# Kernel optimization log

Measured on AMD Instinct MI355X. Metric: run time of the kernel, lower is better.

The kernel has to match this reference:

```python
import jax, jax.numpy as jnp
import numpy as np

N_NODES = 500_000
N_EDGES = 1_000_000
N_GRAPHS = 5_000
NUM_SHAPES = 16
NUM_COLORS = 16
NUM_REL = 3
NUM_CLASS = 10


def setup_inputs() -> dict:
    key = jax.random.key(0)
    ks = jax.random.split(key, 16)
    s = 0.1
    inp = {
        "x": jax.random.randint(ks[0], (N_NODES, 2), 0, NUM_SHAPES, dtype=jnp.int32),
        "edge_index": jax.random.randint(ks[1], (2, N_EDGES), 0, N_NODES, dtype=jnp.int32),
        "edge_type": jax.random.randint(ks[2], (N_EDGES,), 0, NUM_REL, dtype=jnp.int32),
        "ptr": jnp.arange(0, N_NODES + 1, N_NODES // N_GRAPHS, dtype=jnp.int32),  # [G+1]
        "shape_emb": jax.random.normal(ks[3], (NUM_SHAPES, 8), jnp.float32) * s,
        "color_emb": jax.random.normal(ks[4], (NUM_COLORS, 8), jnp.float32) * s,
        "pre_w": jax.random.normal(ks[5], (16, 32), jnp.float32) * s,
        "pre_b": jnp.zeros((32,), jnp.float32),
        "w1_rel": jax.random.normal(ks[6], (NUM_REL, 32, 64), jnp.float32) * s,
        "w1_root": jax.random.normal(ks[7], (32, 64), jnp.float32) * s,
        "b1": jnp.zeros((64,), jnp.float32),
        "w2_rel": jax.random.normal(ks[8], (NUM_REL, 64, 64), jnp.float32) * s,
        "w2_root": jax.random.normal(ks[9], (64, 64), jnp.float32) * s,
        "b2": jnp.zeros((64,), jnp.float32),
        "cls_w": jax.random.normal(ks[10], (64, NUM_CLASS), jnp.float32) * s,
        "cls_b": jnp.zeros((NUM_CLASS,), jnp.float32),
    }
    return inp


def rgcn_layer(h, w_rel, w_root, b, src, dst, etype):
    # PyG RGCNConv: out_i = bias + x_i @ root + sum_r mean_{j in N_r(i)} x_j @ W_r
    n = h.shape[0]
    hr = jnp.einsum('ni,rio->rno', h, w_rel)          # [R, N, F_out]: per-relation transform
    msg = hr[etype, src]                              # [E, F_out]: gather per-edge message
    seg = etype * n + dst                             # relation-separated segment ids
    agg = jax.ops.segment_sum(msg, seg, num_segments=NUM_REL * n)
    cnt = jax.ops.segment_sum(jnp.ones((msg.shape[0],), h.dtype), seg, num_segments=NUM_REL * n)
    agg = (agg / jnp.maximum(cnt, 1.0)[:, None]).reshape(NUM_REL, n, -1).sum(0)
    return agg + h @ w_root + b


def reference(x, edge_index, edge_type, ptr, shape_emb, color_emb, pre_w, pre_b,
              w1_rel, w1_root, b1, w2_rel, w2_root, b2, cls_w, cls_b):
    src, dst = edge_index[0], edge_index[1]
    h = jnp.concatenate([shape_emb[x[:, 0]], color_emb[x[:, 1]]], axis=1)  # [N,16]
    h = jax.nn.relu(h @ pre_w + pre_b)                                     # [N,32]
    h = jax.nn.relu(rgcn_layer(h, w1_rel, w1_root, b1, src, dst, edge_type))
    h = jax.nn.relu(rgcn_layer(h, w2_rel, w2_root, b2, src, dst, edge_type))
    last_idx = ptr[1:] - 1                                                 # [G]
    return h[last_idx] @ cls_w + cls_b                                     # [G, num_class]
```

## Files before the change

### kernel.cpp

```cpp
#include <hip/hip_runtime.h>

#define NB     64
#define CS     16
#define CAP1   32768
#define BC1    (CAP1 / NB)
#define ROWCAP 20
#define PMASK  0xFFFFF
#define CTRB(b) ((b) * CS)

__device__ __forceinline__ int bittest(const unsigned* bm, int n) {
    return (bm[n >> 5] >> (n & 31)) & 1u;
}

__device__ __forceinline__ void claim1(int n, int* __restrict__ slot1,
                                       int* __restrict__ ctr, int bucket,
                                       const int* __restrict__ x,
                                       int* __restrict__ snode) {
    if (atomicCAS(&slot1[n], -1, -2) == -1) {
        int p = atomicAdd(&ctr[CTRB(bucket)], 1);
        if (p < BC1) {
            int sl = bucket * BC1 + p;
            snode[sl] = x[2 * n] | (x[2 * n + 1] << 4);
            atomicExch(&slot1[n], sl);
        }
    }
}

__global__ void scan1_k(const int* __restrict__ src, const int* __restrict__ dst,
                        const int* __restrict__ et, const int* __restrict__ x,
                        int* __restrict__ slot1, int* __restrict__ snode,
                        int* __restrict__ pgE, int* __restrict__ ecnt2,
                        unsigned* __restrict__ bitN1, int* __restrict__ ctr,
                        int nE, int G, unsigned long long M, int stride) {
    int tid = blockIdx.x * blockDim.x + threadIdx.x;
    int nT  = gridDim.x * blockDim.x;
    for (int g = tid; g < G; g += nT) {
        int last = (g + 1) * stride - 1;
        atomicOr(&bitN1[last >> 5], 1u << (last & 31));
        claim1(last, slot1, ctr, g & (NB - 1), x, snode);
    }
    int bucket = (tid >> 6) & (NB - 1);
    int nC = (nE + 3) >> 2;
    for (int c = tid; c < nC; c += nT) {
        int e0 = c * 4;
        int d[4];
        int cnt = min(4, nE - e0);
        if (cnt == 4) { int4 v = *(const int4*)(dst + e0); d[0]=v.x; d[1]=v.y; d[2]=v.z; d[3]=v.w; }
        else for (int k = 0; k < cnt; k++) d[k] = dst[e0 + k];
#pragma unroll
        for (int k = 0; k < 4; k++) {
            if (k >= cnt) break;
            unsigned dk = (unsigned)d[k];
            unsigned q = (unsigned)(((unsigned long long)dk * M) >> 42);
            if ((int)(dk - q * (unsigned)stride) == stride - 1) {
                int e = e0 + k;
                int s = src[e], r = et[e];
                int idx = atomicAdd(&ecnt2[q], 1);
                if (idx < ROWCAP) pgE[q * ROWCAP + idx] = s | (r << 20);
                atomicOr(&bitN1[s >> 5], 1u << (s & 31));
                claim1(s, slot1, ctr, bucket, x, snode);
            }
        }
    }
}

__global__ void scan2_k(const int* __restrict__ src, const int* __restrict__ dst,
                        const int* __restrict__ et, const int* __restrict__ x,
                        const unsigned* __restrict__ bitN1,
                        const int* __restrict__ slot1, int* __restrict__ psE,
                        int* __restrict__ ecnt1, int nE) {
    int tid = blockIdx.x * blockDim.x + threadIdx.x;
    int nT  = gridDim.x * blockDim.x;
    int nC = (nE + 3) >> 2;
    for (int c = tid; c < nC; c += nT) {
        int e0 = c * 4;
        int d[4];
        int cnt = min(4, nE - e0);
        if (cnt == 4) { int4 v = *(const int4*)(dst + e0); d[0]=v.x; d[1]=v.y; d[2]=v.z; d[3]=v.w; }
        else for (int k = 0; k < cnt; k++) d[k] = dst[e0 + k];
#pragma unroll
        for (int k = 0; k < 4; k++) {
            if (k >= cnt) break;
            if (bittest(bitN1, d[k])) {
                int e = e0 + k;
                int s1 = slot1[d[k]];
                if (s1 >= 0) {
                    int s = src[e];
                    int pk = et[e] | (x[2 * s] << 4) | (x[2 * s + 1] << 8);
                    int idx = atomicAdd(&ecnt1[s1], 1);
                    if (idx < ROWCAP) psE[s1 * ROWCAP + idx] = pk;
                }
            }
        }
    }
}

__device__ __forceinline__ float h0_of(int x0, int x1, int fh,
        const float* __restrict__ s_se, const float* __restrict__ s_ce,
        const float* __restrict__ s_pw, const float* __restrict__ s_pb) {
    float h0 = s_pb[fh];
#pragma unroll
    for (int k = 0; k < 8; k++)
        h0 += s_se[x0 * 8 + k] * s_pw[k * 32 + fh] +
              s_ce[x1 * 8 + k] * s_pw[(k + 8) * 32 + fh];
    return fmaxf(h0, 0.f);
}

__device__ __forceinline__ void edge_acc(int pk, int fh,
        const float* __restrict__ s_se, const float* __restrict__ s_ce,
        const float* __restrict__ s_pw, const float* __restrict__ s_pb,
        float& a0, float& a1, float& a2, int& c0, int& c1, int& c2) {
    int r = pk & 15, x0 = (pk >> 4) & 15, x1 = (pk >> 8) & 15;
    float h0 = h0_of(x0, x1, fh, s_se, s_ce, s_pw, s_pb);
    if (r == 0)      { a0 += h0; c0++; }
    else if (r == 1) { a1 += h0; c1++; }
    else             { a2 += h0; c2++; }
}

__global__ __launch_bounds__(256, 2) void h1_k(
        const int* __restrict__ snode, const int* __restrict__ psE,
        const int* __restrict__ ecnt1, const int* __restrict__ ctr,
        const float* __restrict__ se, const float* __restrict__ ce,
        const float* __restrict__ pw, const float* __restrict__ pb,
        const float* __restrict__ w1r, const float* __restrict__ wroot1,
        const float* __restrict__ b1, float* __restrict__ h1buf) {
    __shared__ float smem[9056];
    int t = threadIdx.x;
    for (int i = t; i < 6144; i += 256) smem[i] = w1r[i];
    for (int i = t; i < 2048; i += 256) smem[6144 + i] = wroot1[i];
    if (t < 128) { smem[8192 + t] = se[t]; smem[8320 + t] = ce[t]; }
    for (int i = t; i < 512; i += 256) smem[8448 + i] = pw[i];
    if (t < 32) smem[8960 + t] = pb[t];
    if (t < 64) smem[8992 + t] = b1[t];
    __syncthreads();
    const float* s_w1  = smem;
    const float* s_wr1 = smem + 6144;
    const float* s_se  = smem + 8192;
    const float* s_ce  = smem + 8320;
    const float* s_pw  = smem + 8448;
    const float* s_pb  = smem + 8960;
    const float* s_b1  = smem + 8992;
    int f = t & 63, fh = f & 31;
    int wv  = (blockIdx.x * blockDim.x + t) >> 6;
    int nwv = (gridDim.x * blockDim.x) >> 6;
    int b   = wv & (NB - 1);
    int nj  = nwv >> 6;
    int cnt = min(ctr[CTRB(b)], BC1);
    for (int p = wv >> 6; p < cnt; p += nj) {
        int sl = b * BC1 + p;
        int sx = snode[sl];
        int m  = min(ecnt1[sl], ROWCAP);
        int base = sl * ROWCAP;
        float a0 = 0.f, a1 = 0.f, a2 = 0.f;
        int c0 = 0, c1 = 0, c2 = 0;
        if (m > 0) {
            int4 v = *(const int4*)(psE + base);
            edge_acc(v.x, fh, s_se, s_ce, s_pw, s_pb, a0, a1, a2, c0, c1, c2);
            if (m > 1) edge_acc(v.y, fh, s_se, s_ce, s_pw, s_pb, a0, a1, a2, c0, c1, c2);
            if (m > 2) edge_acc(v.z, fh, s_se, s_ce, s_pw, s_pb, a0, a1, a2, c0, c1, c2);
            if (m > 3) edge_acc(v.w, fh, s_se, s_ce, s_pw, s_pb, a0, a1, a2, c0, c1, c2);
            for (int e = 4; e < m; e++)
                edge_acc(psE[base + e], fh, s_se, s_ce, s_pw, s_pb, a0, a1, a2, c0, c1, c2);
        }
        float h0n = h0_of(sx & 15, (sx >> 4) & 15, fh, s_se, s_ce, s_pw, s_pb);
        float acc = s_b1[f];
        for (int k = 0; k < 32; k++)
            acc += __shfl(h0n, k, 64) * s_wr1[k * 64 + f];
        if (c0) {
            a0 *= 1.0f / (float)c0;
            for (int k = 0; k < 32; k++) acc += __shfl(a0, k, 64) * s_w1[k * 64 + f];
        }
        if (c1) {
            a1 *= 1.0f / (float)c1;
            for (int k = 0; k < 32; k++) acc += __shfl(a1, k, 64) * s_w1[2048 + k * 64 + f];
        }
        if (c2) {
            a2 *= 1.0f / (float)c2;
            for (int k = 0; k < 32; k++) acc += __shfl(a2, k, 64) * s_w1[4096 + k * 64 + f];
        }
        h1buf[sl * 64 + f] = fmaxf(acc, 0.f);
    }
}

__global__ __launch_bounds__(256, 2) void final_k(
        const int* __restrict__ slot1, const float* __restrict__ h1buf,
        const float* __restrict__ w2r, const float* __restrict__ wroot2,
        const float* __restrict__ b2, const float* __restrict__ cw,
        const float* __restrict__ cb, const int* __restrict__ pgE,
        const int* __restrict__ ecnt2, float* __restrict__ out,
        int G, int stride) {
    __shared__ float smem[12944];
    int t = threadIdx.x;
    for (int i = t; i < 12288; i += 256) smem[i] = w2r[i];
    for (int i = t; i < 640; i += 256) smem[12288 + i] = cw[i];
    if (t < 16) smem[12928 + t] = (t < 10) ? cb[t] : 0.f;
    __syncthreads();
    const float* s_w2 = smem;
    const float* s_cw = smem + 12288;
    const float* s_cb = smem + 12928;
    int f = t & 63;
    int g = (blockIdx.x * blockDim.x + t) >> 6;
    if (g >= G) return;
    int last = (g + 1) * stride - 1;
    int sll = slot1[last];
    float hlast = (sll >= 0) ? h1buf[sll * 64 + f] : 0.f;
    int m2 = min(ecnt2[g], ROWCAP);
    float a0 = 0.f, a1 = 0.f, a2 = 0.f;
    int c0 = 0, c1 = 0, c2 = 0;
    if (m2 > 0) {
        int4 v = *(const int4*)(pgE + g * ROWCAP);
        int q0 = slot1[v.x & PMASK];
        int q1 = (m2 > 1) ? slot1[v.y & PMASK] : -1;
        int q2 = (m2 > 2) ? slot1[v.z & PMASK] : -1;
        int q3 = (m2 > 3) ? slot1[v.w & PMASK] : -1;
        float h0v = (q0 >= 0) ? h1buf[q0 * 64 + f] : 0.f;
        float h1v = (q1 >= 0) ? h1buf[q1 * 64 + f] : 0.f;
        float h2v = (q2 >= 0) ? h1buf[q2 * 64 + f] : 0.f;
        float h3v = (q3 >= 0) ? h1buf[q3 * 64 + f] : 0.f;
        { int r = v.x >> 20;
          if (r == 0) { a0 += h0v; c0++; } else if (r == 1) { a1 += h0v; c1++; } else { a2 += h0v; c2++; } }
        if (m2 > 1) { int r = v.y >> 20;
          if (r == 0) { a0 += h1v; c0++; } else if (r == 1) { a1 += h1v; c1++; } else { a2 += h1v; c2++; } }
        if (m2 > 2) { int r = v.z >> 20;
          if (r == 0) { a0 += h2v; c0++; } else if (r == 1) { a1 += h2v; c1++; } else { a2 += h2v; c2++; } }
        if (m2 > 3) { int r = v.w >> 20;
          if (r == 0) { a0 += h3v; c0++; } else if (r == 1) { a1 += h3v; c1++; } else { a2 += h3v; c2++; } }
        for (int e = 4; e < m2; e++) {
            int pk = pgE[g * ROWCAP + e];
            int ss = slot1[pk & PMASK];
            float hv = (ss >= 0) ? h1buf[ss * 64 + f] : 0.f;
            int r = pk >> 20;
            if (r == 0) { a0 += hv; c0++; } else if (r == 1) { a1 += hv; c1++; } else { a2 += hv; c2++; }
        }
    }
    float acc = b2[f];
    for (int k = 0; k < 64; k++)
        acc += __shfl(hlast, k, 64) * wroot2[k * 64 + f];
    if (c0) {
        a0 *= 1.0f / (float)c0;
        for (int k = 0; k < 64; k++) acc += __shfl(a0, k, 64) * s_w2[k * 64 + f];
    }
    if (c1) {
        a1 *= 1.0f / (float)c1;
        for (int k = 0; k < 64; k++) acc += __shfl(a1, k, 64) * s_w2[4096 + k * 64 + f];
    }
    if (c2) {
        a2 *= 1.0f / (float)c2;
        for (int k = 0; k < 64; k++) acc += __shfl(a2, k, 64) * s_w2[8192 + k * 64 + f];
    }
    float h2 = fmaxf(acc, 0.0f);
    float o = (f < 10) ? s_cb[f] : 0.f;
    for (int k = 0; k < 64; k++) {
        float hv = __shfl(h2, k, 64);
        if (f < 10) o += hv * s_cw[k * 10 + f];
    }
    if (f < 10) out[g * 10 + f] = o;
}

static inline size_t rnd(size_t x) { return (x + 255) & ~(size_t)255; }

extern "C" void kernel_launch(void* const* d_in, const int* in_sizes, int n_in,
                              void* d_out, int out_size, void* d_ws, size_t ws_size,
                              hipStream_t stream) {
    const int*   x    = (const int*)d_in[0];
    const int*   ei   = (const int*)d_in[1];
    const int*   et   = (const int*)d_in[2];
    const float* se   = (const float*)d_in[4];
    const float* ce   = (const float*)d_in[5];
    const float* pw   = (const float*)d_in[6];
    const float* pb   = (const float*)d_in[7];
    const float* w1r  = (const float*)d_in[8];
    const float* w1rt = (const float*)d_in[9];
    const float* b1   = (const float*)d_in[10];
    const float* w2r  = (const float*)d_in[11];
    const float* w2rt = (const float*)d_in[12];
    const float* b2   = (const float*)d_in[13];
    const float* cw   = (const float*)d_in[14];
    const float* cb   = (const float*)d_in[15];
    float* out = (float*)d_out;

    const int nN = in_sizes[0] / 2;
    const int nE = in_sizes[2];
    const int G  = in_sizes[3] - 1;
    const int nBW = (nN + 31) / 32;

    const int* src = ei;
    const int* dst = ei + nE;

    const int stride = nN / G;
    const unsigned long long M =
        ((1ULL << 42) + (unsigned long long)stride - 1) / (unsigned long long)stride;

    char* p = (char*)d_ws;
    size_t off = 0;
    auto take = [&](size_t bytes) { size_t o = off; off += rnd(bytes); return o; };

    int*      ctr   = (int*)     (p + take(NB * CS * sizeof(int)));
    unsigned* bitN1 = (unsigned*)(p + take((size_t)nBW * 4));
    int*      ecnt1 = (int*)     (p + take((size_t)CAP1 * 4));
    int*      ecnt2 = (int*)     (p + take((size_t)G * 4));
    size_t zero_bytes = off;
    int*      slot1 = (int*)     (p + take((size_t)nN * 4));
    size_t ff_off = zero_bytes, ff_bytes = off - zero_bytes;
    int*      snode = (int*)     (p + take((size_t)CAP1 * 4));
    int*      psE   = (int*)     (p + take((size_t)CAP1 * ROWCAP * 4));
    int*      pgE   = (int*)     (p + take((size_t)G * ROWCAP * 4));
    float*    h1buf = (float*)   (p + take((size_t)CAP1 * 64 * 4));

    hipMemsetAsync(p, 0, zero_bytes, stream);
    hipMemsetAsync(p + ff_off, 0xFF, ff_bytes, stream);

    int nT = (nE + 3) / 4;
    scan1_k<<<(nT + 255) / 256, 256, 0, stream>>>(src, dst, et, x, slot1, snode,
                                                  pgE, ecnt2, bitN1, ctr, nE, G, M, stride);
    scan2_k<<<(nT + 255) / 256, 256, 0, stream>>>(src, dst, et, x, bitN1, slot1,
                                                  psE, ecnt1, nE);
    h1_k<<<1024, 256, 0, stream>>>(snode, psE, ecnt1, ctr, se, ce, pw, pb,
                                   w1r, w1rt, b1, h1buf);
    final_k<<<(G + 3) / 4, 256, 0, stream>>>(slot1, h1buf, w2r, w2rt, b2, cw, cb,
                                             pgE, ecnt2, out, G, stride);
}
```

Baseline: 180.6 us.

## Shift slot encoding to drop 0xFF memset, stage matvecs via LDS, prefetch rows

The slot table now stores slot+1 so a single zero memset covers it, and the separate 0xFF memset is removed. In both the layer-1 and final kernels, the per-wave matrix-vector products no longer use 32/64 shuffles per weight row. Each wave writes its input vectors to shared memory and reads them back as float4, with four independent accumulators. The layer-1 kernel software-prefetches the next node's metadata, and the final kernel becomes grid-stride with 512 blocks and wroot2 staged in LDS. Weight loads into shared memory are vectorised, at the cost of more LDS per block, which may lower occupancy.

```diff
diff --git a/kernel.cpp b/kernel.cpp
--- a/kernel.cpp
+++ b/kernel.cpp
@@ -16,12 +16,12 @@
                                        int* __restrict__ ctr, int bucket,
                                        const int* __restrict__ x,
                                        int* __restrict__ snode) {
-    if (atomicCAS(&slot1[n], -1, -2) == -1) {
+    if (atomicCAS(&slot1[n], 0, -1) == 0) {
         int p = atomicAdd(&ctr[CTRB(bucket)], 1);
         if (p < BC1) {
             int sl = bucket * BC1 + p;
             snode[sl] = x[2 * n] | (x[2 * n + 1] << 4);
-            atomicExch(&slot1[n], sl);
+            atomicExch(&slot1[n], sl + 1);
         }
     }
 }
@@ -83,7 +83,7 @@
             if (k >= cnt) break;
             if (bittest(bitN1, d[k])) {
                 int e = e0 + k;
-                int s1 = slot1[d[k]];
+                int s1 = slot1[d[k]] - 1;
                 if (s1 >= 0) {
                     int s = src[e];
                     int pk = et[e] | (x[2 * s] << 4) | (x[2 * s + 1] << 8);
@@ -95,10 +95,10 @@
     }
 }
 
-__device__ __forceinline__ float h0_of(int x0, int x1, int fh,
+__device__ __forceinline__ float h0_of(int x0, int x1, int fh, float pbv,
         const float* __restrict__ s_se, const float* __restrict__ s_ce,
-        const float* __restrict__ s_pw, const float* __restrict__ s_pb) {
-    float h0 = s_pb[fh];
+        const float* __restrict__ s_pw) {
+    float h0 = pbv;
 #pragma unroll
     for (int k = 0; k < 8; k++)
         h0 += s_se[x0 * 8 + k] * s_pw[k * 32 + fh] +
@@ -106,15 +106,43 @@
     return fmaxf(h0, 0.f);
 }
 
-__device__ __forceinline__ void edge_acc(int pk, int fh,
+__device__ __forceinline__ void edge_acc(int pk, int fh, float pbv,
         const float* __restrict__ s_se, const float* __restrict__ s_ce,
-        const float* __restrict__ s_pw, const float* __restrict__ s_pb,
+        const float* __restrict__ s_pw,
         float& a0, float& a1, float& a2, int& c0, int& c1, int& c2) {
     int r = pk & 15, x0 = (pk >> 4) & 15, x1 = (pk >> 8) & 15;
-    float h0 = h0_of(x0, x1, fh, s_se, s_ce, s_pw, s_pb);
+    float h0 = h0_of(x0, x1, fh, pbv, s_se, s_ce, s_pw);
     if (r == 0)      { a0 += h0; c0++; }
     else if (r == 1) { a1 += h0; c1++; }
     else             { a2 += h0; c2++; }
+}
+
+__device__ __forceinline__ float mm32(const float* __restrict__ sa,
+                                      const float* __restrict__ w, int f) {
+    float s0 = 0.f, s1 = 0.f, s2 = 0.f, s3 = 0.f;
+#pragma unroll
+    for (int k = 0; k < 32; k += 4) {
+        float4 a = *(const float4*)(sa + k);
+        s0 += a.x * w[(k + 0) * 64 + f];
+        s1 += a.y * w[(k + 1) * 64 + f];
+        s2 += a.z * w[(k + 2) * 64 + f];
+        s3 += a.w * w[(k + 3) * 64 + f];
+    }
+    return (s0 + s1) + (s2 + s3);
+}
+
+__device__ __forceinline__ float mm64(const float* __restrict__ sa,
+                                      const float* __restrict__ w, int f) {
+    float s0 = 0.f, s1 = 0.f, s2 = 0.f, s3 = 0.f;
+#pragma unroll
+    for (int k = 0; k < 64; k += 4) {
+        float4 a = *(const float4*)(sa + k);
+        s0 += a.x * w[(k + 0) * 64 + f];
+        s1 += a.y * w[(k + 1) * 64 + f];
+        s2 += a.z * w[(k + 2) * 64 + f];
+        s3 += a.w * w[(k + 3) * 64 + f];
+    }
+    return (s0 + s1) + (s2 + s3);
 }
 
 __global__ __launch_bounds__(256, 2) void h1_k(
@@ -124,61 +152,71 @@
         const float* __restrict__ pw, const float* __restrict__ pb,
         const float* __restrict__ w1r, const float* __restrict__ wroot1,
         const float* __restrict__ b1, float* __restrict__ h1buf) {
-    __shared__ float smem[9056];
+    __shared__ __align__(16) float smem[9472];
     int t = threadIdx.x;
-    for (int i = t; i < 6144; i += 256) smem[i] = w1r[i];
-    for (int i = t; i < 2048; i += 256) smem[6144 + i] = wroot1[i];
-    if (t < 128) { smem[8192 + t] = se[t]; smem[8320 + t] = ce[t]; }
-    for (int i = t; i < 512; i += 256) smem[8448 + i] = pw[i];
-    if (t < 32) smem[8960 + t] = pb[t];
-    if (t < 64) smem[8992 + t] = b1[t];
+    float4* s4 = (float4*)smem;
+    for (int i = t; i < 1536; i += 256) s4[i] = ((const float4*)w1r)[i];
+    for (int i = t; i < 512;  i += 256) s4[1536 + i] = ((const float4*)wroot1)[i];
+    if (t < 32)       s4[2048 + t] = ((const float4*)se)[t];
+    else if (t < 64)  s4[2048 + t] = ((const float4*)ce)[t - 32];
+    if (t < 128) s4[2112 + t] = ((const float4*)pw)[t];
     __syncthreads();
     const float* s_w1  = smem;
     const float* s_wr1 = smem + 6144;
     const float* s_se  = smem + 8192;
     const float* s_ce  = smem + 8320;
     const float* s_pw  = smem + 8448;
-    const float* s_pb  = smem + 8960;
-    const float* s_b1  = smem + 8992;
-    int f = t & 63, fh = f & 31;
-    int wv  = (blockIdx.x * blockDim.x + t) >> 6;
-    int nwv = (gridDim.x * blockDim.x) >> 6;
+    float* sv = smem + 8960 + (t >> 6) * 128;
+    int lane = t & 63, f = lane, fh = f & 31;
+    float bias1 = b1[f];
+    float pbv   = pb[fh];
+    int wv  = (blockIdx.x << 2) + (t >> 6);
+    int nwv = gridDim.x << 2;
     int b   = wv & (NB - 1);
     int nj  = nwv >> 6;
     int cnt = min(ctr[CTRB(b)], BC1);
-    for (int p = wv >> 6; p < cnt; p += nj) {
-        int sl = b * BC1 + p;
-        int sx = snode[sl];
-        int m  = min(ecnt1[sl], ROWCAP);
-        int base = sl * ROWCAP;
+    int p = wv >> 6;
+    if (p >= cnt) return;
+    int sl = b * BC1 + p;
+    int sx = snode[sl];
+    int m  = min(ecnt1[sl], ROWCAP);
+    int4 v = *(const int4*)(psE + (size_t)sl * ROWCAP);
+    while (true) {
+        int pn = p + nj;
+        bool more = pn < cnt;
+        int sxn = 0, mn = 0; int4 vn = make_int4(0, 0, 0, 0);
+        if (more) {
+            int sln = b * BC1 + pn;
+            sxn = snode[sln];
+            mn  = min(ecnt1[sln], ROWCAP);
+            vn  = *(const int4*)(psE + (size_t)sln * ROWCAP);
+        }
         float a0 = 0.f, a1 = 0.f, a2 = 0.f;
         int c0 = 0, c1 = 0, c2 = 0;
         if (m > 0) {
-            int4 v = *(const int4*)(psE + base);
-            edge_acc(v.x, fh, s_se, s_ce, s_pw, s_pb, a0, a1, a2, c0, c1, c2);
-            if (m > 1) edge_acc(v.y, fh, s_se, s_ce, s_pw, s_pb, a0, a1, a2, c0, c1, c2);
-            if (m > 2) edge_acc(v.z, fh, s_se, s_ce, s_pw, s_pb, a0, a1, a2, c0, c1, c2);
-            if (m > 3) edge_acc(v.w, fh, s_se, s_ce, s_pw, s_pb, a0, a1, a2, c0, c1, c2);
+            edge_acc(v.x, fh, pbv, s_se, s_ce, s_pw, a0, a1, a2, c0, c1, c2);
+            if (m > 1) edge_acc(v.y, fh, pbv, s_se, s_ce, s_pw, a0, a1, a2, c0, c1, c2);
+            if (m > 2) edge_acc(v.z, fh, pbv, s_se, s_ce, s_pw, a0, a1, a2, c0, c1, c2);
+            if (m > 3) edge_acc(v.w, fh, pbv, s_se, s_ce, s_pw, a0, a1, a2, c0, c1, c2);
             for (int e = 4; e < m; e++)
-                edge_acc(psE[base + e], fh, s_se, s_ce, s_pw, s_pb, a0, a1, a2, c0, c1, c2);
-        }
-        float h0n = h0_of(sx & 15, (sx >> 4) & 15, fh, s_se, s_ce, s_pw, s_pb);
-        float acc = s_b1[f];
-        for (int k = 0; k < 32; k++)
-            acc += __shfl(h0n, k, 64) * s_wr1[k * 64 + f];
-        if (c0) {
-            a0 *= 1.0f / (float)c0;
-            for (int k = 0; k < 32; k++) acc += __shfl(a0, k, 64) * s_w1[k * 64 + f];
-        }
-        if (c1) {
-            a1 *= 1.0f / (float)c1;
-            for (int k = 0; k < 32; k++) acc += __shfl(a1, k, 64) * s_w1[2048 + k * 64 + f];
-        }
-        if (c2) {
-            a2 *= 1.0f / (float)c2;
-            for (int k = 0; k < 32; k++) acc += __shfl(a2, k, 64) * s_w1[4096 + k * 64 + f];
-        }
-        h1buf[sl * 64 + f] = fmaxf(acc, 0.f);
+                edge_acc(psE[(size_t)sl * ROWCAP + e], fh, pbv, s_se, s_ce, s_pw,
+                         a0, a1, a2, c0, c1, c2);
+        }
+        float h0n = h0_of(sx & 15, (sx >> 4) & 15, fh, pbv, s_se, s_ce, s_pw);
+        if (lane < 32) {
+            sv[fh]      = h0n;
+            sv[32 + fh] = c0 ? a0 * (1.0f / (float)c0) : 0.f;
+        } else {
+            sv[64 + fh] = c1 ? a1 * (1.0f / (float)c1) : 0.f;
+            sv[96 + fh] = c2 ? a2 * (1.0f / (float)c2) : 0.f;
+        }
+        float acc = bias1 + mm32(sv, s_wr1, f);
+        if (c0) acc += mm32(sv + 32, s_w1, f);
+        if (c1) acc += mm32(sv + 64, s_w1 + 2048, f);
+        if (c2) acc += mm32(sv + 96, s_w1 + 4096, f);
+        h1buf[(size_t)sl * 64 + f] = fmaxf(acc, 0.f);
+        if (!more) break;
+        p = pn; sl = b * BC1 + p; sx = sxn; m = mn; v = vn;
     }
 }
 
@@ -189,72 +227,75 @@
         const float* __restrict__ cb, const int* __restrict__ pgE,
         const int* __restrict__ ecnt2, float* __restrict__ out,
         int G, int stride) {
-    __shared__ float smem[12944];
+    __shared__ __align__(16) float smem[18048];
     int t = threadIdx.x;
-    for (int i = t; i < 12288; i += 256) smem[i] = w2r[i];
-    for (int i = t; i < 640; i += 256) smem[12288 + i] = cw[i];
-    if (t < 16) smem[12928 + t] = (t < 10) ? cb[t] : 0.f;
+    float4* s4 = (float4*)smem;
+    for (int i = t; i < 3072; i += 256) s4[i] = ((const float4*)w2r)[i];
+    for (int i = t; i < 1024; i += 256) s4[3072 + i] = ((const float4*)wroot2)[i];
+    if (t < 160) s4[4096 + t] = ((const float4*)cw)[t];
     __syncthreads();
-    const float* s_w2 = smem;
-    const float* s_cw = smem + 12288;
-    const float* s_cb = smem + 12928;
+    const float* s_w2  = smem;
+    const float* s_wr2 = smem + 12288;
+    const float* s_cw  = smem + 16384;
+    float* sv = smem + 17024 + (t >> 6) * 256;
     int f = t & 63;
-    int g = (blockIdx.x * blockDim.x + t) >> 6;
-    if (g >= G) return;
-    int last = (g + 1) * stride - 1;
-    int sll = slot1[last];
-    float hlast = (sll >= 0) ? h1buf[sll * 64 + f] : 0.f;
-    int m2 = min(ecnt2[g], ROWCAP);
-    float a0 = 0.f, a1 = 0.f, a2 = 0.f;
-    int c0 = 0, c1 = 0, c2 = 0;
-    if (m2 > 0) {
-        int4 v = *(const int4*)(pgE + g * ROWCAP);
-        int q0 = slot1[v.x & PMASK];
-        int q1 = (m2 > 1) ? slot1[v.y & PMASK] : -1;
-        int q2 = (m2 > 2) ? slot1[v.z & PMASK] : -1;
-        int q3 = (m2 > 3) ? slot1[v.w & PMASK] : -1;
-        float h0v = (q0 >= 0) ? h1buf[q0 * 64 + f] : 0.f;
-        float h1v = (q1 >= 0) ? h1buf[q1 * 64 + f] : 0.f;
-        float h2v = (q2 >= 0) ? h1buf[q2 * 64 + f] : 0.f;
-        float h3v = (q3 >= 0) ? h1buf[q3 * 64 + f] : 0.f;
-        { int r = v.x >> 20;
-          if (r == 0) { a0 += h0v; c0++; } else if (r == 1) { a1 += h0v; c1++; } else { a2 += h0v; c2++; } }
-        if (m2 > 1) { int r = v.y >> 20;
-          if (r == 0) { a0 += h1v; c0++; } else if (r == 1) { a1 += h1v; c1++; } else { a2 += h1v; c2++; } }
-        if (m2 > 2) { int r = v.z >> 20;
-          if (r == 0) { a0 += h2v; c0++; } else if (r == 1) { a1 += h2v; c1++; } else { a2 += h2v; c2++; } }
-        if (m2 > 3) { int r = v.w >> 20;
-          if (r == 0) { a0 += h3v; c0++; } else if (r == 1) { a1 += h3v; c1++; } else { a2 += h3v; c2++; } }
-        for (int e = 4; e < m2; e++) {
-            int pk = pgE[g * ROWCAP + e];
-            int ss = slot1[pk & PMASK];
-            float hv = (ss >= 0) ? h1buf[ss * 64 + f] : 0.f;
-            int r = pk >> 20;
-            if (r == 0) { a0 += hv; c0++; } else if (r == 1) { a1 += hv; c1++; } else { a2 += hv; c2++; }
-        }
-    }
-    float acc = b2[f];
-    for (int k = 0; k < 64; k++)
-        acc += __shfl(hlast, k, 64) * wroot2[k * 64 + f];
-    if (c0) {
-        a0 *= 1.0f / (float)c0;
-        for (int k = 0; k < 64; k++) acc += __shfl(a0, k, 64) * s_w2[k * 64 + f];
-    }
-    if (c1) {
-        a1 *= 1.0f / (float)c1;
-        for (int k = 0; k < 64; k++) acc += __shfl(a1, k, 64) * s_w2[4096 + k * 64 + f];
-    }
-    if (c2) {
-        a2 *= 1.0f / (float)c2;
-        for (int k = 0; k < 64; k++) acc += __shfl(a2, k, 64) * s_w2[8192 + k * 64 + f];
-    }
-    float h2 = fmaxf(acc, 0.0f);
-    float o = (f < 10) ? s_cb[f] : 0.f;
-    for (int k = 0; k < 64; k++) {
-        float hv = __shfl(h2, k, 64);
-        if (f < 10) o += hv * s_cw[k * 10 + f];
-    }
-    if (f < 10) out[g * 10 + f] = o;
+    int fc = (f < 10) ? f : 0;
+    float bias2 = b2[f];
+    float cbv = (f < 10) ? cb[f] : 0.f;
+    int wv  = (blockIdx.x << 2) + (t >> 6);
+    int nwv = gridDim.x << 2;
+    for (int g = wv; g < G; g += nwv) {
+        int last = (g + 1) * stride - 1;
+        int sll = slot1[last] - 1;
+        int m2 = min(ecnt2[g], ROWCAP);
+        float a0 = 0.f, a1 = 0.f, a2 = 0.f;
+        int c0 = 0, c1 = 0, c2 = 0;
+        if (m2 > 0) {
+            int4 v = *(const int4*)(pgE + (size_t)g * ROWCAP);
+            int q0 = slot1[v.x & PMASK] - 1;
+            int q1 = (m2 > 1) ? slot1[v.y & PMASK] - 1 : -1;
+            int q2 = (m2 > 2) ? slot1[v.z & PMASK] - 1 : -1;
+            int q3 = (m2 > 3) ? slot1[v.w & PMASK] - 1 : -1;
+            float h0v = (q0 >= 0) ? h1buf[(size_t)q0 * 64 + f] : 0.f;
+            float h1v = (q1 >= 0) ? h1buf[(size_t)q1 * 64 + f] : 0.f;
+            float h2v = (q2 >= 0) ? h1buf[(size_t)q2 * 64 + f] : 0.f;
+            float h3v = (q3 >= 0) ? h1buf[(size_t)q3 * 64 + f] : 0.f;
+            { int r = v.x >> 20;
+              if (r == 0) { a0 += h0v; c0++; } else if (r == 1) { a1 += h0v; c1++; } else { a2 += h0v; c2++; } }
+            if (m2 > 1) { int r = v.y >> 20;
+              if (r == 0) { a0 += h1v; c0++; } else if (r == 1) { a1 += h1v; c1++; } else { a2 += h1v; c2++; } }
+            if (m2 > 2) { int r = v.z >> 20;
+              if (r == 0) { a0 += h2v; c0++; } else if (r == 1) { a1 += h2v; c1++; } else { a2 += h2v; c2++; } }
+            if (m2 > 3) { int r = v.w >> 20;
+              if (r == 0) { a0 += h3v; c0++; } else if (r == 1) { a1 += h3v; c1++; } else { a2 += h3v; c2++; } }
+            for (int e = 4; e < m2; e++) {
+                int pk = pgE[(size_t)g * ROWCAP + e];
+                int ss = slot1[pk & PMASK] - 1;
+                float hv = (ss >= 0) ? h1buf[(size_t)ss * 64 + f] : 0.f;
+                int r = pk >> 20;
+                if (r == 0) { a0 += hv; c0++; } else if (r == 1) { a1 += hv; c1++; } else { a2 += hv; c2++; }
+            }
+        }
+        float hlast = (sll >= 0) ? h1buf[(size_t)sll * 64 + f] : 0.f;
+        sv[f]       = hlast;
+        sv[64 + f]  = c0 ? a0 * (1.0f / (float)c0) : 0.f;
+        sv[128 + f] = c1 ? a1 * (1.0f / (float)c1) : 0.f;
+        sv[192 + f] = c2 ? a2 * (1.0f / (float)c2) : 0.f;
+        float acc = bias2 + mm64(sv, s_wr2, f);
+        if (c0) acc += mm64(sv + 64,  s_w2, f);
+        if (c1) acc += mm64(sv + 128, s_w2 + 4096, f);
+        if (c2) acc += mm64(sv + 192, s_w2 + 8192, f);
+        float h2 = fmaxf(acc, 0.0f);
+        sv[f] = h2;
+        float o = cbv;
+#pragma unroll
+        for (int k = 0; k < 64; k += 4) {
+            float4 a = *(const float4*)(sv + k);
+            o += a.x * s_cw[(k + 0) * 10 + fc] + a.y * s_cw[(k + 1) * 10 + fc]
+               + a.z * s_cw[(k + 2) * 10 + fc] + a.w * s_cw[(k + 3) * 10 + fc];
+        }
+        if (f < 10) out[g * 10 + f] = o;
+    }
 }
 
 static inline size_t rnd(size_t x) { return (x + 255) & ~(size_t)255; }
@@ -299,16 +340,14 @@
     unsigned* bitN1 = (unsigned*)(p + take((size_t)nBW * 4));
     int*      ecnt1 = (int*)     (p + take((size_t)CAP1 * 4));
     int*      ecnt2 = (int*)     (p + take((size_t)G * 4));
+    int*      slot1 = (int*)     (p + take((size_t)nN * 4));
     size_t zero_bytes = off;
-    int*      slot1 = (int*)     (p + take((size_t)nN * 4));
-    size_t ff_off = zero_bytes, ff_bytes = off - zero_bytes;
     int*      snode = (int*)     (p + take((size_t)CAP1 * 4));
     int*      psE   = (int*)     (p + take((size_t)CAP1 * ROWCAP * 4));
     int*      pgE   = (int*)     (p + take((size_t)G * ROWCAP * 4));
     float*    h1buf = (float*)   (p + take((size_t)CAP1 * 64 * 4));
 
     hipMemsetAsync(p, 0, zero_bytes, stream);
-    hipMemsetAsync(p + ff_off, 0xFF, ff_bytes, stream);
 
     int nT = (nE + 3) / 4;
     scan1_k<<<(nT + 255) / 256, 256, 0, stream>>>(src, dst, et, x, slot1, snode,
@@ -317,6 +356,6 @@
                                                   psE, ecnt1, nE);
     h1_k<<<1024, 256, 0, stream>>>(snode, psE, ecnt1, ctr, se, ce, pw, pb,
                                    w1r, w1rt, b1, h1buf);
-    final_k<<<(G + 3) / 4, 256, 0, stream>>>(slot1, h1buf, w2r, w2rt, b2, cw, cb,
-                                             pgE, ecnt2, out, G, stride);
-}
+    final_k<<<512, 256, 0, stream>>>(slot1, h1buf, w2r, w2rt, b2, cw, cb,
+                                     pgE, ecnt2, out, G, stride);
+}
```

After: 162.3 us. -10.1%, faster.
